# Performance work log

Hardware: AMD Instinct MI355X
Metric: run time of the kernel (lower is better)

## Reference

```python
import jax, jax.numpy as jnp
import numpy as np

DIM = 96       # d_model / channels
DSTATE = 16    # SSM state size N
DINNER = 2 * DIM   # expand=2 -> 192
DTRANK = 6     # ceil(DIM/16)
K = 4          # scan directions
B, H, W = 2, 56, 56


def _ln(x, g, b, eps=1e-5):
    m = x.mean(-1, keepdims=True)
    v = x.var(-1, keepdims=True)
    return (x - m) * jax.lax.rsqrt(v + eps) * g + b


def _dwconv3(x, w, b):  # x [B,C,H,W], w [C,1,3,3] depthwise, SAME padding
    y = jax.lax.conv_general_dilated(x, w, (1, 1), [(1, 1), (1, 1)],
                                     feature_group_count=x.shape[1],
                                     dimension_numbers=('NCHW', 'OIHW', 'NCHW'))
    return y + b[None, :, None, None]


def _bn(x, g, b, m, v, eps=1e-5):  # eval-mode BatchNorm2d on NCHW
    inv = jax.lax.rsqrt(v + eps)
    return (x - m[None, :, None, None]) * (inv * g)[None, :, None, None] + b[None, :, None, None]


def _selective_scan(u, dt, A, Bs, Cs, Dp, dt_bias):
    # u, dt: [B,K,D,L]; A: [K,D,N]; Bs,Cs: [B,K,N,L]; Dp, dt_bias: [K,D]
    dt = jax.nn.softplus(dt + dt_bias[None, :, :, None])
    dA = jnp.exp(jnp.einsum('bkdl,kdn->lbkdn', dt, A))           # [L,B,K,D,N]
    dBu = jnp.einsum('bkdl,bknl,bkdl->lbkdn', dt, Bs, u)          # [L,B,K,D,N]
    Ct = jnp.moveaxis(Cs, -1, 0)                                  # [L,B,K,N]
    h0 = jnp.zeros(dA.shape[1:], dA.dtype)

    def step(h, inp):
        dA_l, dBu_l, C_l = inp
        h = dA_l * h + dBu_l
        return h, jnp.einsum('bkdn,bkn->bkd', h, C_l)

    _, ys = jax.lax.scan(step, h0, (dA, dBu, Ct))                 # ys [L,B,K,D]
    return jnp.moveaxis(ys, 0, -1) + u * Dp[None, :, :, None]     # [B,K,D,L]


def setup_inputs() -> dict:
    key = jax.random.key(0)
    ks = jax.random.split(key, 12)
    s = 0.02
    f32 = jnp.float32
    inp = {}
    inp['x'] = jax.random.normal(ks[0], (B, H, W, DIM), f32)
    # conv branch: depthwise 3x3 + BN + ReLU + 1x1 + BN
    inp['dw_w'] = jax.random.normal(ks[1], (DIM, 1, 3, 3), f32) * s
    inp['dw_b'] = jnp.zeros((DIM,), f32)
    inp['bn1_g'] = jnp.ones((DIM,), f32); inp['bn1_b'] = jnp.zeros((DIM,), f32)
    inp['bn1_m'] = jnp.zeros((DIM,), f32); inp['bn1_v'] = jnp.ones((DIM,), f32)
    inp['pw_w'] = jax.random.normal(ks[2], (DIM, DIM), f32) * s
    inp['pw_b'] = jnp.zeros((DIM,), f32)
    inp['bn2_g'] = jnp.ones((DIM,), f32); inp['bn2_b'] = jnp.zeros((DIM,), f32)
    inp['bn2_m'] = jnp.zeros((DIM,), f32); inp['bn2_v'] = jnp.ones((DIM,), f32)
    # pre-mamba LayerNorm
    inp['ln_g'] = jnp.ones((DIM,), f32); inp['ln_b'] = jnp.zeros((DIM,), f32)
    # SS2D params
    inp['in_proj_w'] = jax.random.normal(ks[3], (2 * DINNER, DIM), f32) * s
    inp['conv_w'] = jax.random.normal(ks[4], (DINNER, 1, 3, 3), f32) * s
    inp['conv_b'] = jnp.zeros((DINNER,), f32)
    inp['x_proj_w'] = jax.random.normal(ks[5], (K, DTRANK + 2 * DSTATE, DINNER), f32) * s
    inp['dt_w'] = jax.random.normal(ks[6], (K, DINNER, DTRANK), f32) * s
    inp['dt_b'] = jnp.full((K, DINNER), -4.6, f32)  # softplus(dt_b) ~= 0.01
    inp['A_logs'] = jnp.log(jnp.tile(jnp.arange(1, DSTATE + 1, dtype=f32), (K * DINNER, 1)))
    inp['Ds'] = jnp.ones((K * DINNER,), f32)
    inp['out_norm_g'] = jnp.ones((DINNER,), f32); inp['out_norm_b'] = jnp.zeros((DINNER,), f32)
    inp['out_proj_w'] = jax.random.normal(ks[7], (DIM, DINNER), f32) * s
    # fusion: Linear(2*dim, dim) + LayerNorm(dim)
    inp['fus_w'] = jax.random.normal(ks[8], (DIM, 2 * DIM), f32) * s
    inp['fus_b'] = jnp.zeros((DIM,), f32)
    inp['fus_ln_g'] = jnp.ones((DIM,), f32); inp['fus_ln_b'] = jnp.zeros((DIM,), f32)
    return inp


def reference(x, dw_w, dw_b, bn1_g, bn1_b, bn1_m, bn1_v, pw_w, pw_b,
              bn2_g, bn2_b, bn2_m, bn2_v, ln_g, ln_b,
              in_proj_w, conv_w, conv_b, x_proj_w, dt_w, dt_b, A_logs, Ds,
              out_norm_g, out_norm_b, out_proj_w, fus_w, fus_b, fus_ln_g, fus_ln_b):
    Bsz, Hh, Ww, C = x.shape
    L = Hh * Ww
    # ----- conv branch -----
    xc = jnp.transpose(x, (0, 3, 1, 2))                       # [B,C,H,W]
    c = jax.nn.relu(_bn(_dwconv3(xc, dw_w, dw_b), bn1_g, bn1_b, bn1_m, bn1_v))
    c = jnp.einsum('bchw,oc->bohw', c, pw_w) + pw_b[None, :, None, None]
    conv_out = jnp.transpose(_bn(c, bn2_g, bn2_b, bn2_m, bn2_v), (0, 2, 3, 1))
    # ----- mamba (SS2D) branch -----
    xn = _ln(x, ln_g, ln_b)
    xz = xn @ in_proj_w.T                                     # [B,H,W,2*Din]
    xm, z = jnp.split(xz, 2, axis=-1)
    xm = jnp.transpose(xm, (0, 3, 1, 2))                      # [B,Din,H,W]
    xm = jax.nn.silu(_dwconv3(xm, conv_w, conv_b))
    v1 = xm.reshape(Bsz, DINNER, L)                           # row-major scan
    v2 = jnp.transpose(xm, (0, 1, 3, 2)).reshape(Bsz, DINNER, L)  # col-major scan
    xs = jnp.stack([v1, v2, v1[..., ::-1], v2[..., ::-1]], axis=1)  # [B,4,Din,L]
    x_dbl = jnp.einsum('bkdl,kcd->bkcl', xs, x_proj_w)
    dts, Bmat, Cmat = jnp.split(x_dbl, [DTRANK, DTRANK + DSTATE], axis=2)
    dts = jnp.einsum('bkrl,kdr->bkdl', dts, dt_w)
    A = -jnp.exp(A_logs).reshape(K, DINNER, DSTATE)
    out_y = _selective_scan(xs, dts, A, Bmat, Cmat, Ds.reshape(K, DINNER), dt_b)
    y1 = out_y[:, 0]
    inv_y = out_y[:, 2:4][..., ::-1]
    y2 = inv_y[:, 0]
    y3 = jnp.transpose(inv_y[:, 1].reshape(Bsz, DINNER, Ww, Hh), (0, 1, 3, 2)).reshape(Bsz, DINNER, L)
    y4 = jnp.transpose(out_y[:, 1].reshape(Bsz, DINNER, Ww, Hh), (0, 1, 3, 2)).reshape(Bsz, DINNER, L)
    y = jnp.transpose(y1 + y2 + y3 + y4, (0, 2, 1)).reshape(Bsz, Hh, Ww, DINNER)
    y = _ln(y, out_norm_g, out_norm_b)
    y = y * jax.nn.silu(z)
    mamba_out = y @ out_proj_w.T                              # [B,H,W,C]
    # ----- fusion + residual -----
    fused = jnp.concatenate([conv_out, mamba_out], axis=-1) @ fus_w.T + fus_b
    fused = _ln(fused, fus_ln_g, fus_ln_b)
    return x + fused
```

## Files before the change

### kernel.cpp

```cpp
#include <hip/hip_runtime.h>
#include <math.h>

#define BZ 2
#define HH 56
#define WW 56
#define LL 3136
#define CC 96
#define DI 192
#define NS 16
#define RR 6
#define NT 49
#define NCH 98
#define CH 32

#define OFF_CONV   0
#define OFF_XMRAW  602112
#define OFF_Z      1806336
#define OFF_V1     3010560
#define OFF_V2     4214784
#define OFF_DT     5419008
#define OFF_BS     10235904
#define OFF_CS     10637312
#define OFF_Y      11038720
#define OFF_Y13    15855616
#define OFF_T      18264064
#define OFF_W2     19468288

__device__ __forceinline__ float softplusf(float x) {
    if (x > 20.f) return x;
    return log1pf(__expf(x));
}

__global__ __launch_bounds__(64) void k0_w2(const float* __restrict__ fus_w,
                                            const float* __restrict__ opw,
                                            float* __restrict__ W2) {
    int i = blockIdx.x * 64 + threadIdx.x;
    if (i >= CC * DI) return;
    int o = i / DI, d = i % DI;
    float acc = 0.f;
    for (int j = 0; j < CC; ++j)
        acc += fus_w[o * DI + CC + j] * opw[j * DI + d];
    W2[i] = acc;
}

__global__ __launch_bounds__(256) void k0c_negA(const float* __restrict__ A_logs,
                                                float* __restrict__ negA) {
    int i = blockIdx.x * 256 + threadIdx.x;
    if (i < 4 * DI * NS) negA[i] = -__expf(A_logs[i]);
}

__global__ __launch_bounds__(256) void k1a_dw(const float* __restrict__ x,
    const float* __restrict__ dw_w, const float* __restrict__ dw_b,
    const float* __restrict__ bn1_g, const float* __restrict__ bn1_b,
    const float* __restrict__ bn1_m, const float* __restrict__ bn1_v,
    float* __restrict__ cbuf) {
    int i = blockIdx.x * 256 + threadIdx.x;
    if (i >= BZ * LL * CC) return;
    int c = i % CC;
    int bl = i / CC;
    int l = bl % LL, b = bl / LL;
    int h = l / WW, w = l % WW;
    float acc = dw_b[c];
    #pragma unroll
    for (int dy = -1; dy <= 1; ++dy) {
        int hh = h + dy; if (hh < 0 || hh >= HH) continue;
        #pragma unroll
        for (int dx = -1; dx <= 1; ++dx) {
            int ww = w + dx; if (ww < 0 || ww >= WW) continue;
            acc += x[((b * HH + hh) * WW + ww) * CC + c] * dw_w[c * 9 + (dy + 1) * 3 + (dx + 1)];
        }
    }
    float inv = rsqrtf(bn1_v[c] + 1e-5f);
    float v = (acc - bn1_m[c]) * inv * bn1_g[c] + bn1_b[c];
    cbuf[i] = fmaxf(v, 0.f);
}

__global__ __launch_bounds__(256) void k1b_pw(const float* __restrict__ cbuf,
    const float* __restrict__ pw_w, const float* __restrict__ pw_b,
    const float* __restrict__ bn2_g, const float* __restrict__ bn2_b,
    const float* __restrict__ bn2_m, const float* __restrict__ bn2_v,
    float* __restrict__ conv_out) {
    int t0 = blockIdx.x * 64;
    int og = blockIdx.y;
    int b = blockIdx.z;
    int lane = threadIdx.x & 63;
    int wvu = __builtin_amdgcn_readfirstlane(threadIdx.x >> 6);
    __shared__ float ct[CC * 65];
    __shared__ float res[64 * 49];
    const float* cb = cbuf + (b * LL + t0) * CC;
    for (int e = threadIdx.x; e < 64 * CC; e += 256) {
        int p = e / CC, c = e % CC;
        ct[c * 65 + p] = cb[e];
    }
    __syncthreads();
    int o0 = og * 48 + wvu * 12;
    float acc[12];
    const float* pb = pw_b + o0;
    #pragma unroll
    for (int j = 0; j < 12; ++j) acc[j] = pb[j];
    const float* wb = pw_w + o0 * CC;
    for (int c = 0; c < CC; ++c) {
        float xv = ct[c * 65 + lane];
        #pragma unroll
        for (int j = 0; j < 12; ++j)
            acc[j] += xv * wb[j * CC + c];
    }
    #pragma unroll
    for (int j = 0; j < 12; ++j) {
        int o = o0 + j;
        float inv = rsqrtf(bn2_v[o] + 1e-5f);
        res[lane * 49 + wvu * 12 + j] = (acc[j] - bn2_m[o]) * inv * bn2_g[o] + bn2_b[o];
    }
    __syncthreads();
    float* ob = conv_out + (b * LL + t0) * CC + og * 48;
    for (int e = threadIdx.x; e < 64 * 48; e += 256) {
        int pl = e / 48, o = e % 48;
        ob[pl * CC + o] = res[pl * 49 + o];
    }
}

__global__ __launch_bounds__(256) void k2_inproj(const float* __restrict__ x,
    const float* __restrict__ ln_g, const float* __restrict__ ln_b,
    const float* __restrict__ ipw,
    float* __restrict__ xm_raw, float* __restrict__ z_buf) {
    int t0 = blockIdx.x * 64;
    int og = blockIdx.y;
    int b = blockIdx.z;
    int lane = threadIdx.x & 63;
    int wv = threadIdx.x >> 6;
    int wvu = __builtin_amdgcn_readfirstlane(wv);
    __shared__ float xt[64 * 97];
    __shared__ float xn[96 * 65];
    __shared__ float ps[4][64], ps2[4][64];
    const float* xb = x + (b * LL + t0) * CC;
    for (int e = threadIdx.x; e < 64 * CC; e += 256) {
        int p = e / CC, c = e % CC;
        xt[p * 97 + c] = xb[e];
    }
    __syncthreads();
    float s = 0.f, s2 = 0.f;
    #pragma unroll
    for (int j = 0; j < 24; ++j) {
        float v = xt[lane * 97 + wvu * 24 + j];
        s += v; s2 += v * v;
    }
    ps[wv][lane] = s; ps2[wv][lane] = s2;
    __syncthreads();
    float st = 0.f, st2 = 0.f;
    #pragma unroll
    for (int i = 0; i < 4; ++i) { st += ps[i][lane]; st2 += ps2[i][lane]; }
    float m = st * (1.f / 96.f);
    float inv = rsqrtf(st2 * (1.f / 96.f) - m * m + 1e-5f);
    #pragma unroll
    for (int j = 0; j < 24; ++j) {
        int c = wvu * 24 + j;
        xn[c * 65 + lane] = (xt[lane * 97 + c] - m) * inv * ln_g[c] + ln_b[c];
    }
    __syncthreads();
    float acc[12];
    #pragma unroll
    for (int j = 0; j < 12; ++j) acc[j] = 0.f;
    int o0 = og * 48 + wvu * 12;
    const float* wbase = ipw + o0 * CC;
    for (int c = 0; c < CC; ++c) {
        float xv = xn[c * 65 + lane];
        #pragma unroll
        for (int j = 0; j < 12; ++j)
            acc[j] += xv * wbase[j * CC + c];
    }
    int p = t0 + lane;
    #pragma unroll
    for (int j = 0; j < 12; ++j) {
        int out = o0 + j;
        if (out < DI) xm_raw[(b * DI + out) * LL + p] = acc[j];
        else          z_buf[(b * DI + (out - DI)) * LL + p] = acc[j];
    }
}

__global__ __launch_bounds__(256) void k3_dw(const float* __restrict__ xm_raw,
    const float* __restrict__ conv_w, const float* __restrict__ conv_b,
    float* __restrict__ v1, float* __restrict__ v2) {
    int bd = blockIdx.x;
    int half = blockIdx.y;
    int d = bd % DI;
    int h0 = half * 28;
    __shared__ float tile[28 * 57];
    const float* src = xm_raw + bd * LL;
    float wloc[9];
    #pragma unroll
    for (int i = 0; i < 9; ++i) wloc[i] = conv_w[d * 9 + i];
    float bias = conv_b[d];
    for (int e = threadIdx.x; e < 28 * WW; e += 256) {
        int hl = e / WW, w = e % WW;
        int h = h0 + hl;
        float acc = bias;
        #pragma unroll
        for (int dy = -1; dy <= 1; ++dy) {
            int hh = h + dy; if (hh < 0 || hh >= HH) continue;
            #pragma unroll
            for (int dx = -1; dx <= 1; ++dx) {
                int ww = w + dx; if (ww < 0 || ww >= WW) continue;
                acc += src[hh * WW + ww] * wloc[(dy + 1) * 3 + (dx + 1)];
            }
        }
        float sig = 1.f / (1.f + __expf(-acc));
        float v = acc * sig;
        v1[bd * LL + h * WW + w] = v;
        tile[hl * 57 + w] = v;
    }
    __syncthreads();
    for (int e = threadIdx.x; e < 28 * WW; e += 256) {
        int w = e / 28, hl = e % 28;
        v2[bd * LL + w * HH + h0 + hl] = tile[hl * 57 + w];
    }
}

__global__ __launch_bounds__(256) void k4a_xproj(const float* __restrict__ v1,
    const float* __restrict__ v2, const float* __restrict__ xpw,
    float* __restrict__ dtr_g, float* __restrict__ B_s, float* __restrict__ C_s) {
    int tile = blockIdx.x;
    int k = blockIdx.y, b = blockIdx.z;
    int lane = threadIdx.x & 63;
    int wvu = __builtin_amdgcn_readfirstlane(threadIdx.x >> 6);
    int t0 = tile * 64;
    int r0 = wvu * 10; if (r0 > 28) r0 = 28;
    const float* src = ((k & 1) == 0 ? v1 : v2) + b * DI * LL + t0;
    float acc[10];
    #pragma unroll
    for (int i = 0; i < 10; ++i) acc[i] = 0.f;
    const float* wbase = xpw + (k * 38 + r0) * DI;
    for (int d = 0; d < DI; ++d) {
        float xv = src[d * LL + lane];
        #pragma unroll
        for (int i = 0; i < 10; ++i)
            acc[i] += xv * wbase[i * DI + d];
    }
    int bk = b * 4 + k;
    int p = t0 + lane;
    #pragma unroll
    for (int i = 0; i < 10; ++i) {
        int c = r0 + i;
        if (c < RR) {
            dtr_g[(bk * RR + c) * LL + p] = acc[i];
        } else if (c < RR + NS) {
            B_s[(bk * NS + (c - RR)) * LL + p] = acc[i];
        } else {
            C_s[(bk * NS + (c - RR - NS)) * LL + p] = acc[i];
        }
    }
}

__global__ __launch_bounds__(256) void k4b_dt(const float* __restrict__ dtr_g,
    const float* __restrict__ dtw, const float* __restrict__ dtb,
    float* __restrict__ dt_s) {
    int t0 = blockIdx.x * 64;
    int k = blockIdx.y, b = blockIdx.z;
    int lane = threadIdx.x & 63;
    int wvu = __builtin_amdgcn_readfirstlane(threadIdx.x >> 6);
    int bk = b * 4 + k;
    int p = t0 + lane;
    float r[RR];
    #pragma unroll
    for (int i = 0; i < RR; ++i) r[i] = dtr_g[(bk * RR + i) * LL + p];
    for (int i = 0; i < 48; ++i) {
        int d = wvu * 48 + i;
        float a = dtb[k * DI + d];
        const float* wr = dtw + (k * DI + d) * RR;
        #pragma unroll
        for (int q = 0; q < RR; ++q)
            a += r[q] * wr[q];
        dt_s[(bk * DI + d) * LL + p] = softplusf(a);
    }
}

__global__ __launch_bounds__(128, 4) void k5a_scan(const float* __restrict__ dt_s,
    const float* __restrict__ B_s, const float* __restrict__ C_s,
    const float* __restrict__ v1, const float* __restrict__ v2,
    const float* __restrict__ A_logs, float* __restrict__ y_scan,
    float* __restrict__ hl_buf, float* __restrict__ Tbuf) {
    int bx = blockIdx.x;
    int dg = bx % 3, c = bx / 3;
    int k = blockIdx.y, b = blockIdx.z;
    int bk = b * 4 + k;
    int tid = threadIdx.x;
    int lane = tid & 63;
    int wvu = __builtin_amdgcn_readfirstlane(tid >> 6);
    int d0 = dg * 64, d = d0 + lane;
    bool fwd = (k < 2);
    int s0 = fwd ? c * CH : (LL - (c + 1) * CH);
    __shared__ float dtl[64 * 32];
    __shared__ float ul[64 * 32];
    __shared__ alignas(16) float bc[32 * 32];
    float Ae[8];
    const float* ap = A_logs + (k * DI + d) * NS + wvu * 8;
    #pragma unroll
    for (int n = 0; n < 8; ++n) Ae[n] = -__expf(ap[n]) * 1.442695040888963f;
    const float* dtp = dt_s + (bk * DI + d0) * LL + s0;
    const float* up  = ((k & 1) == 0 ? v1 : v2) + (b * DI + d0) * LL + s0;
    #pragma unroll
    for (int q = 0; q < 4; ++q) {
        int e = q * 128 + tid;
        int row = e >> 3;
        int p4 = (e & 7) << 2;
        float4 dv = *(const float4*)(dtp + row * LL + p4);
        float4 uv = *(const float4*)(up + row * LL + p4);
        float dvv[4] = {dv.x, dv.y, dv.z, dv.w};
        float uvv[4] = {uv.x, uv.y, uv.z, uv.w};
        int rsw = row & 31;
        #pragma unroll
        for (int t = 0; t < 4; ++t) {
            int s = fwd ? (p4 + t) : (31 - (p4 + t));
            dtl[row * 32 + (s ^ rsw)] = dvv[t];
            ul [row * 32 + (s ^ rsw)] = dvv[t] * uvv[t];
        }
    }
    #pragma unroll
    for (int q = 0; q < 2; ++q) {
        int e = q * 128 + tid;
        int row = e >> 3;
        int p4 = (e & 7) << 2;
        const float* src = (row < 16 ? B_s + (bk * NS + row) * LL
                                     : C_s + (bk * NS + (row - 16)) * LL) + s0 + p4;
        float4 v = *(const float4*)src;
        float vv[4] = {v.x, v.y, v.z, v.w};
        #pragma unroll
        for (int t = 0; t < 4; ++t) {
            int s = fwd ? (p4 + t) : (31 - (p4 + t));
            bc[s * 32 + (row ^ ((s & 7) << 2))] = vv[t];
        }
    }
    __syncthreads();
    float h[8];
    #pragma unroll
    for (int n = 0; n < 8; ++n) h[n] = 0.f;
    float cum = 0.f;
    int lbase = lane * 32;
    int lsw = lane & 31;
    int w8 = wvu * 8;
    #pragma unroll
    for (int seg = 0; seg < 4; ++seg) {
        float yv_[8];
        #pragma unroll
        for (int jj = 0; jj < 8; ++jj) {
            int j = seg * 8 + jj;
            float dtv = dtl[lbase + (j ^ lsw)];
            float du  = ul [lbase + (j ^ lsw)];
            cum += dtv;
            int cswz = (j & 7) << 2;
            const float* rb0 = &bc[j * 32 + ( w8       ^ cswz)];
            const float* rb1 = &bc[j * 32 + ((w8 +  4) ^ cswz)];
            const float* rc0 = &bc[j * 32 + ((w8 + 16) ^ cswz)];
            const float* rc1 = &bc[j * 32 + ((w8 + 20) ^ cswz)];
            float4 b0 = *(const float4*)rb0, b1 = *(const float4*)rb1;
            float4 c0 = *(const float4*)rc0, c1 = *(const float4*)rc1;
            float bv[8] = {b0.x, b0.y, b0.z, b0.w, b1.x, b1.y, b1.z, b1.w};
            float cv[8] = {c0.x, c0.y, c0.z, c0.w, c1.x, c1.y, c1.z, c1.w};
            float y = 0.f;
            #pragma unroll
            for (int n = 0; n < 8; ++n) {
                h[n] = exp2f(dtv * Ae[n]) * h[n] + du * bv[n];
                y += h[n] * cv[n];
            }
            yv_[jj] = y;
        }
        __syncthreads();
        float* dst = (wvu == 0) ? dtl : ul;
        #pragma unroll
        for (int jj = 0; jj < 8; ++jj) {
            int j = seg * 8 + jj;
            dst[lbase + (j ^ lsw)] = yv_[jj];
        }
    }
    __syncthreads();
    float* yp = y_scan + (bk * DI + d0) * LL + s0;
    #pragma unroll
    for (int q = 0; q < 4; ++q) {
        int e = q * 128 + tid;
        int row = e >> 3;
        int p4 = (e & 7) << 2;
        int rsw = row & 31;
        float ov[4];
        #pragma unroll
        for (int t = 0; t < 4; ++t) {
            int s = fwd ? (p4 + t) : (31 - (p4 + t));
            ov[t] = dtl[row * 32 + (s ^ rsw)] + ul[row * 32 + (s ^ rsw)];
        }
        *(float4*)(yp + row * LL + p4) = make_float4(ov[0], ov[1], ov[2], ov[3]);
    }
    float4* hp4 = (float4*)(hl_buf + (bk * NCH + c) * (DI * NS) + d * NS + wvu * 8);
    hp4[0] = make_float4(h[0], h[1], h[2], h[3]);
    hp4[1] = make_float4(h[4], h[5], h[6], h[7]);
    if (wvu == 0) Tbuf[(bk * NCH + c) * DI + d] = cum;
}

__global__ __launch_bounds__(64) void k5c_comb(float* __restrict__ hl_buf,
    const float* __restrict__ Tbuf, const float* __restrict__ negA) {
    int dg = blockIdx.x, k = blockIdx.y, b = blockIdx.z;
    int lane = threadIdx.x, dl = lane >> 4, n = lane & 15;
    int d = dg * 4 + dl;
    int bk = b * 4 + k;
    const int HS = DI * NS;
    float Av = negA[(k * DI + d) * NS + n];
    float* hp = hl_buf + (bk * NCH) * HS + dg * 64 + lane;
    const float* Tp = Tbuf + (bk * NCH) * DI + d;
    float hl[8], T[8];
    #pragma unroll
    for (int i = 0; i < 8; ++i) { hl[i] = hp[i * HS]; T[i] = Tp[i * DI]; }
    float H = 0.f;
    for (int cb = 0; cb < 96; cb += 8) {
        #pragma unroll
        for (int i = 0; i < 8; ++i) {
            int c = cb + i;
            float hlv = hl[i], Tv = T[i];
            int nc = c + 8;
            if (nc < NCH) { hl[i] = hp[nc * HS]; T[i] = Tp[nc * DI]; }
            hp[c * HS] = H;
            H = hlv + __expf(Av * Tv) * H;
        }
    }
    hp[96 * HS] = H;
    H = hl[0] + __expf(Av * T[0]) * H;
    hp[97 * HS] = H;
}

__global__ __launch_bounds__(256) void k5d_corr(const float* __restrict__ dtr_g,
    const float* __restrict__ dtw, const float* __restrict__ dtb,
    const float* __restrict__ C_s, const float* __restrict__ hin,
    const float* __restrict__ negA, float* __restrict__ y_scan) {
    int t = blockIdx.x;
    int k = blockIdx.y, b = blockIdx.z;
    bool fwd = (k < 2);
    int c  = fwd ? (t + 1) : (NCH - 1 - t);
    int s0 = fwd ? (t + 1) * CH : t * CH;
    int p32 = threadIdx.x & 31, sl = threadIdx.x >> 5;
    int bk = b * 4 + k;
    __shared__ float c_l[16 * 33];
    for (int e = threadIdx.x; e < 16 * CH; e += 256) {
        int n = e >> 5, s = e & 31;
        c_l[n * 33 + s] = C_s[(bk * NS + n) * LL + s0 + s];
    }
    const float* rp = dtr_g + (bk * RR) * LL + s0 + p32;
    float r[RR];
    #pragma unroll
    for (int q = 0; q < RR; ++q) r[q] = rp[q * LL];
    __syncthreads();
    for (int j = 0; j < 24; ++j) {
        int d = sl * 24 + j;
        int dd = k * DI + d;
        const float* wr = dtw + dd * RR;
        float a = dtb[dd];
        #pragma unroll
        for (int q = 0; q < RR; ++q)
            a += r[q] * wr[q];
        float dtv = softplusf(a);
        float cum = dtv;
        if (fwd) {
            #pragma unroll
            for (int off = 1; off < 32; off <<= 1) {
                float o = __shfl_up(cum, off, 32);
                if (p32 >= off) cum += o;
            }
        } else {
            #pragma unroll
            for (int off = 1; off < 32; off <<= 1) {
                float o = __shfl_down(cum, off, 32);
                if (p32 < 32 - off) cum += o;
            }
        }
        const float* hp = hin + (bk * NCH + c) * (DI * NS) + d * 16;
        const float* ap = negA + (k * DI + d) * NS;
        float acc = 0.f;
        #pragma unroll
        for (int n = 0; n < 16; ++n) {
            acc += c_l[n * 33 + p32] * __expf(ap[n] * cum) * hp[n];
        }
        y_scan[(bk * DI + d) * LL + s0 + p32] += acc;
    }
}

__global__ __launch_bounds__(256) void k5b_tr(const float* __restrict__ y_scan,
                                              float* __restrict__ y13t) {
    int idx = blockIdx.x;
    int d = idx % DI;
    int bk = idx / DI;
    int kk = bk % 2, b = bk / 2;
    int k = (kk == 0) ? 1 : 3;
    __shared__ float tile[HH * 57];
    const float* src = y_scan + ((b * 4 + k) * DI + d) * LL;
    for (int e = threadIdx.x; e < LL; e += 256) {
        int w = e / HH, h = e % HH;
        tile[h * 57 + w] = src[e];
    }
    __syncthreads();
    float* dst = y13t + idx * LL;
    for (int e = threadIdx.x; e < LL; e += 256) {
        int h = e / WW, w = e % WW;
        dst[e] = tile[h * 57 + w];
    }
}

__global__ __launch_bounds__(256) void k6_gather(const float* __restrict__ y_scan,
    const float* __restrict__ y13t, const float* __restrict__ v1,
    const float* __restrict__ z_buf, const float* __restrict__ Ds,
    const float* __restrict__ ong, const float* __restrict__ onb,
    float* __restrict__ t_buf) {
    int t0 = blockIdx.x * 16;
    int b = blockIdx.y;
    int p16 = threadIdx.x & 15, sl = threadIdx.x >> 4;
    int p = t0 + p16;
    __shared__ float yv[DI * 17];
    __shared__ float ps[16][16], ps2[16][16];
    float s = 0.f, s2 = 0.f;
    for (int j = 0; j < 12; ++j) {
        int d = sl * 12 + j;
        float dsum = Ds[d] + Ds[DI + d] + Ds[2 * DI + d] + Ds[3 * DI + d];
        float val = y_scan[((b * 4 + 0) * DI + d) * LL + p]
                  + y_scan[((b * 4 + 2) * DI + d) * LL + p]
                  + y13t[((b * 2 + 0) * DI + d) * LL + p]
                  + y13t[((b * 2 + 1) * DI + d) * LL + p]
                  + v1[(b * DI + d) * LL + p] * dsum;
        yv[d * 17 + p16] = val;
        s += val; s2 += val * val;
    }
    ps[sl][p16] = s; ps2[sl][p16] = s2;
    __syncthreads();
    float st = 0.f, st2 = 0.f;
    #pragma unroll
    for (int i = 0; i < 16; ++i) { st += ps[i][p16]; st2 += ps2[i][p16]; }
    float m = st * (1.f / 192.f);
    float inv = rsqrtf(st2 * (1.f / 192.f) - m * m + 1e-5f);
    for (int j = 0; j < 12; ++j) {
        int d = sl * 12 + j;
        float val = (yv[d * 17 + p16] - m) * inv * ong[d] + onb[d];
        float zz = z_buf[(b * DI + d) * LL + p];
        float sig = 1.f / (1.f + __expf(-zz));
        t_buf[(b * DI + d) * LL + p] = val * zz * sig;
    }
}

__global__ __launch_bounds__(256) void k7a_mm(const float* __restrict__ t_buf,
    const float* __restrict__ conv_out, const float* __restrict__ W2,
    const float* __restrict__ fus_w, const float* __restrict__ fus_b,
    float* __restrict__ fusedT) {
    int t0 = blockIdx.x * 64;
    int og = blockIdx.y;
    int b = blockIdx.z;
    int lane = threadIdx.x & 63;
    int wvu = __builtin_amdgcn_readfirstlane(threadIdx.x >> 6);
    __shared__ float ct[CC * 65];
    const float* cb = conv_out + (b * LL + t0) * CC;
    for (int e = threadIdx.x; e < 64 * CC; e += 256) {
        int p = e / CC, c = e % CC;
        ct[c * 65 + p] = cb[e];
    }
    __syncthreads();
    int o0 = og * 12 + wvu * 3;
    float acc[3];
    #pragma unroll
    for (int j = 0; j < 3; ++j) acc[j] = fus_b[o0 + j];
    int p = t0 + lane;
    const float* w2 = W2 + o0 * DI;
    for (int d = 0; d < DI; ++d) {
        float tv = t_buf[(b * DI + d) * LL + p];
        #pragma unroll
        for (int j = 0; j < 3; ++j)
            acc[j] += tv * w2[j * DI + d];
    }
    const float* fw = fus_w + o0 * DI;
    for (int c = 0; c < CC; ++c) {
        float cv = ct[c * 65 + lane];
        #pragma unroll
        for (int j = 0; j < 3; ++j)
            acc[j] += cv * fw[j * DI + c];
    }
    #pragma unroll
    for (int j = 0; j < 3; ++j)
        fusedT[(b * CC + o0 + j) * LL + p] = acc[j];
}

__global__ __launch_bounds__(256) void k7b_ln(const float* __restrict__ fusedT,
    const float* __restrict__ flg, const float* __restrict__ flb,
    const float* __restrict__ x, float* __restrict__ out) {
    int t0 = blockIdx.x * 16;
    int b = blockIdx.y;
    int p16 = threadIdx.x & 15, sl = threadIdx.x >> 4;
    __shared__ float ft[CC * 17];
    __shared__ float res[16 * 97];
    __shared__ float ps[16][16], ps2[16][16];
    for (int e = threadIdx.x; e < CC * 16; e += 256) {
        int o = e >> 4, p = e & 15;
        ft[o * 17 + p] = fusedT[(b * CC + o) * LL + t0 + p];
    }
    __syncthreads();
    float s = 0.f, s2 = 0.f;
    #pragma unroll
    for (int j = 0; j < 6; ++j) {
        float v = ft[(sl * 6 + j) * 17 + p16];
        s += v; s2 += v * v;
    }
    ps[sl][p16] = s; ps2[sl][p16] = s2;
    __syncthreads();
    float st = 0.f, st2 = 0.f;
    #pragma unroll
    for (int i = 0; i < 16; ++i) { st += ps[i][p16]; st2 += ps2[i][p16]; }
    float m = st * (1.f / 96.f);
    float inv = rsqrtf(st2 * (1.f / 96.f) - m * m + 1e-5f);
    #pragma unroll
    for (int j = 0; j < 6; ++j) {
        int o = sl * 6 + j;
        res[p16 * 97 + o] = (ft[o * 17 + p16] - m) * inv * flg[o] + flb[o];
    }
    __syncthreads();
    const float* xb = x + (b * LL + t0) * CC;
    float* ob = out + (b * LL + t0) * CC;
    for (int e = threadIdx.x; e < 16 * CC; e += 256) {
        int pl = e / CC, o = e % CC;
        ob[e] = xb[e] + res[pl * 97 + o];
    }
}

extern "C" void kernel_launch(void* const* d_in, const int* in_sizes, int n_in,
                              void* d_out, int out_size, void* d_ws, size_t ws_size,
                              hipStream_t stream) {
    const float* x        = (const float*)d_in[0];
    const float* dw_w     = (const float*)d_in[1];
    const float* dw_b     = (const float*)d_in[2];
    const float* bn1_g    = (const float*)d_in[3];
    const float* bn1_b    = (const float*)d_in[4];
    const float* bn1_m    = (const float*)d_in[5];
    const float* bn1_v    = (const float*)d_in[6];
    const float* pw_w     = (const float*)d_in[7];
    const float* pw_b     = (const float*)d_in[8];
    const float* bn2_g    = (const float*)d_in[9];
    const float* bn2_b    = (const float*)d_in[10];
    const float* bn2_m    = (const float*)d_in[11];
    const float* bn2_v    = (const float*)d_in[12];
    const float* ln_g     = (const float*)d_in[13];
    const float* ln_b     = (const float*)d_in[14];
    const float* ipw      = (const float*)d_in[15];
    const float* conv_w   = (const float*)d_in[16];
    const float* conv_b   = (const float*)d_in[17];
    const float* xpw      = (const float*)d_in[18];
    const float* dtw      = (const float*)d_in[19];
    const float* dtb      = (const float*)d_in[20];
    const float* A_logs   = (const float*)d_in[21];
    const float* Ds       = (const float*)d_in[22];
    const float* ong      = (const float*)d_in[23];
    const float* onb      = (const float*)d_in[24];
    const float* opw      = (const float*)d_in[25];
    const float* fus_w    = (const float*)d_in[26];
    const float* fus_b    = (const float*)d_in[27];
    const float* flg      = (const float*)d_in[28];
    const float* flb      = (const float*)d_in[29];

    float* ws = (float*)d_ws;
    float* conv_out = ws + OFF_CONV;
    float* xm_raw   = ws + OFF_XMRAW;
    float* z_buf    = ws + OFF_Z;
    float* v1       = ws + OFF_V1;
    float* v2       = ws + OFF_V2;
    float* dt_s     = ws + OFF_DT;
    float* B_s      = ws + OFF_BS;
    float* C_s      = ws + OFF_CS;
    float* y_scan   = ws + OFF_Y;
    float* y13t     = ws + OFF_Y13;
    float* t_buf    = ws + OFF_T;
    float* W2       = ws + OFF_W2;
    float* cbuf     = y13t;
    float* hl_buf   = y13t;
    float* Tbuf     = xm_raw;
    float* dtr_g    = xm_raw + 262144;
    float* negA     = B_s;
    float* fusedT   = y13t;
    float* out      = (float*)d_out;

    k0_w2<<<dim3((CC * DI + 63) / 64), dim3(64), 0, stream>>>(fus_w, opw, W2);
    k1a_dw<<<dim3((BZ * LL * CC + 255) / 256), dim3(256), 0, stream>>>(x, dw_w, dw_b,
                                                     bn1_g, bn1_b, bn1_m, bn1_v, cbuf);
    k1b_pw<<<dim3(NT, 2, BZ), dim3(256), 0, stream>>>(cbuf, pw_w, pw_b,
                                                   bn2_g, bn2_b, bn2_m, bn2_v, conv_out);
    k2_inproj<<<dim3(NT, 8, BZ), dim3(256), 0, stream>>>(x, ln_g, ln_b, ipw, xm_raw, z_buf);
    k3_dw<<<dim3(BZ * DI, 2), dim3(256), 0, stream>>>(xm_raw, conv_w, conv_b, v1, v2);
    k4a_xproj<<<dim3(NT, 4, BZ), dim3(256), 0, stream>>>(v1, v2, xpw, dtr_g, B_s, C_s);
    k4b_dt<<<dim3(NT, 4, BZ), dim3(256), 0, stream>>>(dtr_g, dtw, dtb, dt_s);
    k5a_scan<<<dim3(3 * NCH, 4, BZ), dim3(128), 0, stream>>>(dt_s, B_s, C_s, v1, v2, A_logs,
                                                             y_scan, hl_buf, Tbuf);
    k0c_negA<<<dim3(48), dim3(256), 0, stream>>>(A_logs, negA);
    k5c_comb<<<dim3(48, 4, BZ), dim3(64), 0, stream>>>(hl_buf, Tbuf, negA);
    k5d_corr<<<dim3(NCH - 1, 4, BZ), dim3(256), 0, stream>>>(dtr_g, dtw, dtb, C_s,
                                                             hl_buf, negA, y_scan);
    k5b_tr<<<dim3(BZ * 2 * DI), dim3(256), 0, stream>>>(y_scan, y13t);
    k6_gather<<<dim3(196, BZ), dim3(256), 0, stream>>>(y_scan, y13t, v1, z_buf, Ds, ong, onb, t_buf);
    k7a_mm<<<dim3(NT, 8, BZ), dim3(256), 0, stream>>>(t_buf, conv_out, W2, fus_w, fus_b, fusedT);
    k7b_ln<<<dim3(196, BZ), dim3(256), 0, stream>>>(fusedT, flg, flb, x, out);
}
```

Before: 367.6 us.

## Fuse conv-branch kernels, fusion matmul with LayerNorm, and weight-prep kernels

Merges the depthwise conv+BN+ReLU kernel into the pointwise conv kernel, so the intermediate activation is built in shared memory instead of a global buffer. Merges the fusion matmul with the final LayerNorm+residual kernel, so each 512-thread block computes all 96 outputs for 64 pixels and normalizes them in place, removing the fusedT round trip. Combines the W2 and negA precompute into one launch and relocates negA into t_buf, which is not written until k6 after the scan kernels that read negA. This removes three launches and two global intermediates, but the fused kernels launch far fewer blocks (98 instead of several hundred), which lowers parallelism on a GPU with many CUs.

```diff
diff --git a/kernel.cpp b/kernel.cpp
--- a/kernel.cpp
+++ b/kernel.cpp
@@ -31,69 +31,59 @@
     return log1pf(__expf(x));
 }
 
-__global__ __launch_bounds__(64) void k0_w2(const float* __restrict__ fus_w,
-                                            const float* __restrict__ opw,
-                                            float* __restrict__ W2) {
-    int i = blockIdx.x * 64 + threadIdx.x;
-    if (i >= CC * DI) return;
-    int o = i / DI, d = i % DI;
-    float acc = 0.f;
-    for (int j = 0; j < CC; ++j)
-        acc += fus_w[o * DI + CC + j] * opw[j * DI + d];
-    W2[i] = acc;
-}
-
-__global__ __launch_bounds__(256) void k0c_negA(const float* __restrict__ A_logs,
-                                                float* __restrict__ negA) {
+__global__ __launch_bounds__(256) void k0_prep(const float* __restrict__ fus_w,
+                                               const float* __restrict__ opw,
+                                               const float* __restrict__ A_logs,
+                                               float* __restrict__ W2,
+                                               float* __restrict__ negA) {
     int i = blockIdx.x * 256 + threadIdx.x;
-    if (i < 4 * DI * NS) negA[i] = -__expf(A_logs[i]);
-}
-
-__global__ __launch_bounds__(256) void k1a_dw(const float* __restrict__ x,
+    if (i < CC * DI) {
+        int o = i / DI, d = i % DI;
+        float acc = 0.f;
+        for (int j = 0; j < CC; ++j)
+            acc += fus_w[o * DI + CC + j] * opw[j * DI + d];
+        W2[i] = acc;
+    } else if (i < CC * DI + 4 * DI * NS) {
+        int j = i - CC * DI;
+        negA[j] = -__expf(A_logs[j]);
+    }
+}
+
+__global__ __launch_bounds__(512) void k1_fused(const float* __restrict__ x,
     const float* __restrict__ dw_w, const float* __restrict__ dw_b,
     const float* __restrict__ bn1_g, const float* __restrict__ bn1_b,
     const float* __restrict__ bn1_m, const float* __restrict__ bn1_v,
-    float* __restrict__ cbuf) {
-    int i = blockIdx.x * 256 + threadIdx.x;
-    if (i >= BZ * LL * CC) return;
-    int c = i % CC;
-    int bl = i / CC;
-    int l = bl % LL, b = bl / LL;
-    int h = l / WW, w = l % WW;
-    float acc = dw_b[c];
-    #pragma unroll
-    for (int dy = -1; dy <= 1; ++dy) {
-        int hh = h + dy; if (hh < 0 || hh >= HH) continue;
-        #pragma unroll
-        for (int dx = -1; dx <= 1; ++dx) {
-            int ww = w + dx; if (ww < 0 || ww >= WW) continue;
-            acc += x[((b * HH + hh) * WW + ww) * CC + c] * dw_w[c * 9 + (dy + 1) * 3 + (dx + 1)];
-        }
-    }
-    float inv = rsqrtf(bn1_v[c] + 1e-5f);
-    float v = (acc - bn1_m[c]) * inv * bn1_g[c] + bn1_b[c];
-    cbuf[i] = fmaxf(v, 0.f);
-}
-
-__global__ __launch_bounds__(256) void k1b_pw(const float* __restrict__ cbuf,
     const float* __restrict__ pw_w, const float* __restrict__ pw_b,
     const float* __restrict__ bn2_g, const float* __restrict__ bn2_b,
     const float* __restrict__ bn2_m, const float* __restrict__ bn2_v,
     float* __restrict__ conv_out) {
     int t0 = blockIdx.x * 64;
-    int og = blockIdx.y;
-    int b = blockIdx.z;
-    int lane = threadIdx.x & 63;
-    int wvu = __builtin_amdgcn_readfirstlane(threadIdx.x >> 6);
+    int b = blockIdx.y;
+    int tid = threadIdx.x;
+    int lane = tid & 63;
+    int wvu = __builtin_amdgcn_readfirstlane(tid >> 6);
     __shared__ float ct[CC * 65];
-    __shared__ float res[64 * 49];
-    const float* cb = cbuf + (b * LL + t0) * CC;
-    for (int e = threadIdx.x; e < 64 * CC; e += 256) {
+    __shared__ float res[64 * 97];
+    for (int e = tid; e < 64 * CC; e += 512) {
         int p = e / CC, c = e % CC;
-        ct[c * 65 + p] = cb[e];
-    }
-    __syncthreads();
-    int o0 = og * 48 + wvu * 12;
+        int l = t0 + p;
+        int h = l / WW, w = l % WW;
+        float acc = dw_b[c];
+        #pragma unroll
+        for (int dy = -1; dy <= 1; ++dy) {
+            int hh = h + dy; if (hh < 0 || hh >= HH) continue;
+            #pragma unroll
+            for (int dx = -1; dx <= 1; ++dx) {
+                int ww = w + dx; if (ww < 0 || ww >= WW) continue;
+                acc += x[((b * HH + hh) * WW + ww) * CC + c] * dw_w[c * 9 + (dy + 1) * 3 + (dx + 1)];
+            }
+        }
+        float inv = rsqrtf(bn1_v[c] + 1e-5f);
+        float v = (acc - bn1_m[c]) * inv * bn1_g[c] + bn1_b[c];
+        ct[c * 65 + p] = fmaxf(v, 0.f);
+    }
+    __syncthreads();
+    int o0 = wvu * 12;
     float acc[12];
     const float* pb = pw_b + o0;
     #pragma unroll
@@ -109,13 +99,13 @@
     for (int j = 0; j < 12; ++j) {
         int o = o0 + j;
         float inv = rsqrtf(bn2_v[o] + 1e-5f);
-        res[lane * 49 + wvu * 12 + j] = (acc[j] - bn2_m[o]) * inv * bn2_g[o] + bn2_b[o];
-    }
-    __syncthreads();
-    float* ob = conv_out + (b * LL + t0) * CC + og * 48;
-    for (int e = threadIdx.x; e < 64 * 48; e += 256) {
-        int pl = e / 48, o = e % 48;
-        ob[pl * CC + o] = res[pl * 49 + o];
+        res[lane * 97 + o] = (acc[j] - bn2_m[o]) * inv * bn2_g[o] + bn2_b[o];
+    }
+    __syncthreads();
+    float* ob = conv_out + (b * LL + t0) * CC;
+    for (int e = tid; e < 64 * CC; e += 512) {
+        int pl = e / CC, o = e % CC;
+        ob[e] = res[pl * 97 + o];
     }
 }
 
@@ -538,82 +528,67 @@
     }
 }
 
-__global__ __launch_bounds__(256) void k7a_mm(const float* __restrict__ t_buf,
+__global__ __launch_bounds__(512) void k7_fused(const float* __restrict__ t_buf,
     const float* __restrict__ conv_out, const float* __restrict__ W2,
     const float* __restrict__ fus_w, const float* __restrict__ fus_b,
-    float* __restrict__ fusedT) {
+    const float* __restrict__ flg, const float* __restrict__ flb,
+    const float* __restrict__ x, float* __restrict__ out) {
     int t0 = blockIdx.x * 64;
-    int og = blockIdx.y;
-    int b = blockIdx.z;
-    int lane = threadIdx.x & 63;
-    int wvu = __builtin_amdgcn_readfirstlane(threadIdx.x >> 6);
+    int b = blockIdx.y;
+    int tid = threadIdx.x;
+    int lane = tid & 63;
+    int wv = tid >> 6;
+    int wvu = __builtin_amdgcn_readfirstlane(wv);
     __shared__ float ct[CC * 65];
+    __shared__ float res[64 * 97];
+    __shared__ float ps[8][64], ps2[8][64];
     const float* cb = conv_out + (b * LL + t0) * CC;
-    for (int e = threadIdx.x; e < 64 * CC; e += 256) {
+    for (int e = tid; e < 64 * CC; e += 512) {
         int p = e / CC, c = e % CC;
         ct[c * 65 + p] = cb[e];
     }
     __syncthreads();
-    int o0 = og * 12 + wvu * 3;
-    float acc[3];
-    #pragma unroll
-    for (int j = 0; j < 3; ++j) acc[j] = fus_b[o0 + j];
+    int o0 = wvu * 12;
+    float acc[12];
+    #pragma unroll
+    for (int j = 0; j < 12; ++j) acc[j] = fus_b[o0 + j];
     int p = t0 + lane;
     const float* w2 = W2 + o0 * DI;
     for (int d = 0; d < DI; ++d) {
         float tv = t_buf[(b * DI + d) * LL + p];
         #pragma unroll
-        for (int j = 0; j < 3; ++j)
+        for (int j = 0; j < 12; ++j)
             acc[j] += tv * w2[j * DI + d];
     }
     const float* fw = fus_w + o0 * DI;
     for (int c = 0; c < CC; ++c) {
         float cv = ct[c * 65 + lane];
         #pragma unroll
-        for (int j = 0; j < 3; ++j)
+        for (int j = 0; j < 12; ++j)
             acc[j] += cv * fw[j * DI + c];
     }
-    #pragma unroll
-    for (int j = 0; j < 3; ++j)
-        fusedT[(b * CC + o0 + j) * LL + p] = acc[j];
-}
-
-__global__ __launch_bounds__(256) void k7b_ln(const float* __restrict__ fusedT,
-    const float* __restrict__ flg, const float* __restrict__ flb,
-    const float* __restrict__ x, float* __restrict__ out) {
-    int t0 = blockIdx.x * 16;
-    int b = blockIdx.y;
-    int p16 = threadIdx.x & 15, sl = threadIdx.x >> 4;
-    __shared__ float ft[CC * 17];
-    __shared__ float res[16 * 97];
-    __shared__ float ps[16][16], ps2[16][16];
-    for (int e = threadIdx.x; e < CC * 16; e += 256) {
-        int o = e >> 4, p = e & 15;
-        ft[o * 17 + p] = fusedT[(b * CC + o) * LL + t0 + p];
-    }
-    __syncthreads();
     float s = 0.f, s2 = 0.f;
     #pragma unroll
-    for (int j = 0; j < 6; ++j) {
-        float v = ft[(sl * 6 + j) * 17 + p16];
-        s += v; s2 += v * v;
-    }
-    ps[sl][p16] = s; ps2[sl][p16] = s2;
+    for (int j = 0; j < 12; ++j) {
+        res[lane * 97 + o0 + j] = acc[j];
+        s += acc[j]; s2 += acc[j] * acc[j];
+    }
+    ps[wv][lane] = s; ps2[wv][lane] = s2;
     __syncthreads();
     float st = 0.f, st2 = 0.f;
     #pragma unroll
-    for (int i = 0; i < 16; ++i) { st += ps[i][p16]; st2 += ps2[i][p16]; }
+    for (int i = 0; i < 8; ++i) { st += ps[i][lane]; st2 += ps2[i][lane]; }
     float m = st * (1.f / 96.f);
     float inv = rsqrtf(st2 * (1.f / 96.f) - m * m + 1e-5f);
     #pragma unroll
-    for (int j = 0; j < 6; ++j) {
-        int o = sl * 6 + j;
-        res[p16 * 97 + o] = (ft[o * 17 + p16] - m) * inv * flg[o] + flb[o];
+    for (int j = 0; j < 12; ++j) {
+        int o = o0 + j;
+        res[lane * 97 + o] = (res[lane * 97 + o] - m) * inv * flg[o] + flb[o];
     }
     __syncthreads();
     const float* xb = x + (b * LL + t0) * CC;
     float* ob = out + (b * LL + t0) * CC;
-    for (int e = threadIdx.x; e < 16 * CC; e += 256) {
+    for (int e = tid; e < 64 * CC; e += 512) {
         int pl = e / CC, o = e % CC;
         ob[e] = xb[e] + res[pl * 97 + o];
     }
@@ -666,31 +641,27 @@
     float* y13t     = ws + OFF_Y13;
     float* t_buf    = ws + OFF_T;
     float* W2       = ws + OFF_W2;
-    float* cbuf     = y13t;
     float* hl_buf   = y13t;
     float* Tbuf     = xm_raw;
     float* dtr_g    = xm_raw + 262144;
-    float* negA     = B_s;
-    float* fusedT   = y13t;
+    float* negA     = t_buf;
     float* out      = (float*)d_out;
 
-    k0_w2<<<dim3((CC * DI + 63) / 64), dim3(64), 0, stream>>>(fus_w, opw, W2);
-    k1a_dw<<<dim3((BZ * LL * CC + 255) / 256), dim3(256), 0, stream>>>(x, dw_w, dw_b,
-                                                     bn1_g, bn1_b, bn1_m, bn1_v, cbuf);
-    k1b_pw<<<dim3(NT, 2, BZ), dim3(256), 0, stream>>>(cbuf, pw_w, pw_b,
-                                                   bn2_g, bn2_b, bn2_m, bn2_v, conv_out);
+    k0_prep<<<dim3((CC * DI + 4 * DI * NS + 255) / 256), dim3(256), 0, stream>>>(
+        fus_w, opw, A_logs, W2, negA);
+    k1_fused<<<dim3(NT, BZ), dim3(512), 0, stream>>>(x, dw_w, dw_b,
+        bn1_g, bn1_b, bn1_m, bn1_v, pw_w, pw_b, bn2_g, bn2_b, bn2_m, bn2_v, conv_out);
     k2_inproj<<<dim3(NT, 8, BZ), dim3(256), 0, stream>>>(x, ln_g, ln_b, ipw, xm_raw, z_buf);
     k3_dw<<<dim3(BZ * DI, 2), dim3(256), 0, stream>>>(xm_raw, conv_w, conv_b, v1, v2);
     k4a_xproj<<<dim3(NT, 4, BZ), dim3(256), 0, stream>>>(v1, v2, xpw, dtr_g, B_s, C_s);
     k4b_dt<<<dim3(NT, 4, BZ), dim3(256), 0, stream>>>(dtr_g, dtw, dtb, dt_s);
     k5a_scan<<<dim3(3 * NCH, 4, BZ), dim3(128), 0, stream>>>(dt_s, B_s, C_s, v1, v2, A_logs,
                                                              y_scan, hl_buf, Tbuf);
-    k0c_negA<<<dim3(48), dim3(256), 0, stream>>>(A_logs, negA);
     k5c_comb<<<dim3(48, 4, BZ), dim3(64), 0, stream>>>(hl_buf, Tbuf, negA);
     k5d_corr<<<dim3(NCH - 1, 4, BZ), dim3(256), 0, stream>>>(dtr_g, dtw, dtb, C_s,
                                                              hl_buf, negA, y_scan);
     k5b_tr<<<dim3(BZ * 2 * DI), dim3(256), 0, stream>>>(y_scan, y13t);
     k6_gather<<<dim3(196, BZ), dim3(256), 0, stream>>>(y_scan, y13t, v1, z_buf, Ds, ong, onb, t_buf);
-    k7a_mm<<<dim3(NT, 8, BZ), dim3(256), 0, stream>>>(t_buf, conv_out, W2, fus_w, fus_b, fusedT);
-    k7b_ln<<<dim3(196, BZ), dim3(256), 0, stream>>>(fusedT, flg, flb, x, out);
-}
+    k7_fused<<<dim3(NT, BZ), dim3(512), 0, stream>>>(t_buf, conv_out, W2, fus_w, fus_b,
+                                                     flg, flb, x, out);
+}
```

Measured after the change: 410.6 us. 11.7% more time.
